# Performance work log

Hardware: AMD Instinct MI355X
Metric: run time of the kernel (lower is better)

The kernel has to match this reference:

```python
import jax, jax.numpy as jnp
import numpy as np

B, Q, C, N_PER, GS = 8, 2048, 256, 64, 8
H1, H2 = 256, 64
EPS = 1e-5


def make_grid():
    a = jnp.linspace(-0.1, 0.1, GS)
    gx, gy = jnp.meshgrid(a, a, indexing='ij')  # torch.meshgrid default 'ij'
    return jnp.stack([gx.reshape(-1), gy.reshape(-1)], axis=1)  # (n, 2)


def setup_inputs() -> dict:
    key = jax.random.key(0)
    ks = jax.random.split(key, 10)
    s = lambda k, shp, fan: jax.random.normal(k, shp, jnp.float32) / np.sqrt(fan)
    return {
        'tokens': jax.random.normal(ks[0], (B, Q, C), jnp.float32),
        'grid': make_grid(),
        'Wc': s(ks[1], (C, 3), C), 'bc': jnp.zeros((3,), jnp.float32),
        'W1': s(ks[2], (C + 2, H1), C + 2), 'b1': jnp.zeros((H1,), jnp.float32),
        'gamma1': jnp.ones((H1,), jnp.float32), 'beta1': jnp.zeros((H1,), jnp.float32),
        'W2': s(ks[3], (H1, H2), H1), 'b2': jnp.zeros((H2,), jnp.float32),
        'gamma2': jnp.ones((H2,), jnp.float32), 'beta2': jnp.zeros((H2,), jnp.float32),
        'W3': s(ks[4], (H2, 3), H2), 'b3': jnp.zeros((3,), jnp.float32),
    }


def batchnorm(x, gamma, beta):
    # BatchNorm1d in training mode: stats over batch (B*Q) and length (n) dims,
    # per channel (last axis here).
    mean = jnp.mean(x, axis=(0, 1, 2), keepdims=True)
    var = jnp.var(x, axis=(0, 1, 2), keepdims=True)
    return gamma * (x - mean) * jax.lax.rsqrt(var + EPS) + beta


def reference(tokens, grid, Wc, bc, W1, b1, gamma1, beta1, W2, b2, gamma2, beta2, W3, b3):
    coarse = tokens @ Wc + bc  # (B, Q, 3)
    # conv1 (1x1) on concat([tokens_expanded, grid]) == split matmul + broadcast add;
    # avoids materializing the (B,Q,n,C+2) concat explicitly.
    tok_part = tokens @ W1[:C]                 # (B, Q, H1)
    grid_part = grid @ W1[C:]                  # (n, H1)
    h = tok_part[:, :, None, :] + grid_part[None, None, :, :] + b1  # (B, Q, n, H1)
    h = jax.nn.relu(batchnorm(h, gamma1, beta1))
    h = jnp.einsum('bqnc,cd->bqnd', h, W2) + b2  # (B, Q, n, H2)
    h = jax.nn.relu(batchnorm(h, gamma2, beta2))
    disp = jnp.einsum('bqnc,cd->bqnd', h, W3) + b3  # (B, Q, n, 3)
    fine = (coarse[:, :, None, :] + disp).reshape(B, Q * N_PER, 3)
    return coarse, fine
```

## Files before the change

### kernel.cpp

```cpp
#include <hip/hip_runtime.h>
#include <hip/hip_bf16.h>

#define ROWS 16384
#define C_   256
#define H1_  256
#define H2_  64
#define EPSN 1e-5f

typedef __bf16 bf16x8 __attribute__((ext_vector_type(8)));
typedef __bf16 bf16x4 __attribute__((ext_vector_type(4)));
typedef float  f32x4  __attribute__((ext_vector_type(4)));

__global__ __launch_bounds__(256) void k0_pack(const float* __restrict__ W1,
                                               const float* __restrict__ W2,
                                               const float* __restrict__ W3,
                                               __bf16* __restrict__ W1p,
                                               __bf16* __restrict__ W2p,
                                               __bf16* __restrict__ W3p,
                                               float* __restrict__ zero_base) {
    int idx = blockIdx.x * 256 + threadIdx.x;
    if (idx < 65536) {
        int j = idx & 7, l = (idx >> 3) & 63, rest = idx >> 9;
        int ks = rest & 7, CT = rest >> 3;
        int k = ks * 32 + ((l >> 4) << 3) + j;
        int c = CT * 16 + (l & 15);
        W1p[idx] = (__bf16)W1[k * H1_ + c];
    } else {
        int i2 = idx - 65536;
        int j = i2 & 7, l = (i2 >> 3) & 63, rest = i2 >> 9;
        int ks = rest & 7, CK = rest >> 3;
        int k = ks * 32 + ((l >> 4) << 3) + j;
        int c2 = CK * 16 + (l & 15);
        W2p[i2] = (__bf16)W2[k * H2_ + c2];
    }
    if (idx < 1024) {
        int j = idx & 7, l = (idx >> 3) & 63, ks = idx >> 9;
        int k = ks * 32 + ((l >> 4) << 3) + j;
        int c = l & 15;
        W3p[idx] = (c < 3) ? (__bf16)W3[k * 3 + c] : (__bf16)0.f;
    }
    if (idx < 24576) zero_base[idx] = 0.0f;
}

__global__ __launch_bounds__(256) void kc(const float* __restrict__ tokens,
                                          const float* __restrict__ Wc,
                                          const float* __restrict__ bc,
                                          float* __restrict__ coarse) {
    int t = threadIdx.x, w = t >> 6, l = t & 63;
    int row = blockIdx.x * 4 + w;
    int c0 = l * 4;
    f32x4 tv = *(const f32x4*)(tokens + (size_t)row * C_ + c0);
    f32x4 w0 = *(const f32x4*)(Wc + c0 * 3);
    f32x4 w1 = *(const f32x4*)(Wc + c0 * 3 + 4);
    f32x4 w2 = *(const f32x4*)(Wc + c0 * 3 + 8);
    float wc[12] = {w0[0], w0[1], w0[2], w0[3], w1[0], w1[1], w1[2], w1[3],
                    w2[0], w2[1], w2[2], w2[3]};
    float p[3] = {0.f, 0.f, 0.f};
#pragma unroll
    for (int i = 0; i < 4; ++i)
#pragma unroll
        for (int j = 0; j < 3; ++j) p[j] = fmaf(tv[i], wc[i * 3 + j], p[j]);
#pragma unroll
    for (int off = 1; off < 64; off <<= 1) {
#pragma unroll
        for (int j = 0; j < 3; ++j) p[j] += __shfl_xor(p[j], off, 64);
    }
    if (l == 0) {
#pragma unroll
        for (int j = 0; j < 3; ++j) coarse[row * 3 + j] = p[j] + bc[j];
    }
}

__global__ __launch_bounds__(256) void k1a(const float* __restrict__ tokens,
                                           const __bf16* __restrict__ W1p,
                                           float* __restrict__ tokpart,
                                           float* __restrict__ p1s,
                                           float* __restrict__ p1q) {
    __shared__ __align__(16) __bf16 Al[16 * 264];
    int t = threadIdx.x, w = t >> 6, l = t & 63;
    int quad = l >> 4, col = l & 15;
    int rowbase = (blockIdx.x >> 1) * 16;
    int colhalf = blockIdx.x & 1;
    int slot = blockIdx.x & 31;

    bf16x8 bfr[16];
#pragma unroll
    for (int ctl = 0; ctl < 2; ++ctl)
#pragma unroll
        for (int ks = 0; ks < 8; ++ks) {
            int CT = colhalf * 8 + w * 2 + ctl;
            bfr[ctl * 8 + ks] = *(const bf16x8*)(W1p + (((CT * 8 + ks) * 64 + l) * 8));
        }

    {
        int r = t >> 4, cb = (t & 15) * 16;
        const float* src = tokens + (size_t)(rowbase + r) * C_ + cb;
        f32x4 t0 = *(const f32x4*)(src);
        f32x4 t1 = *(const f32x4*)(src + 4);
        f32x4 t2 = *(const f32x4*)(src + 8);
        f32x4 t3 = *(const f32x4*)(src + 12);
        bf16x8 v0, v1;
#pragma unroll
        for (int e = 0; e < 4; ++e) {
            v0[e] = (__bf16)t0[e]; v0[e + 4] = (__bf16)t1[e];
            v1[e] = (__bf16)t2[e]; v1[e + 4] = (__bf16)t3[e];
        }
        *(bf16x8*)(&Al[r * 264 + cb]) = v0;
        *(bf16x8*)(&Al[r * 264 + cb + 8]) = v1;
    }
    __syncthreads();

    bf16x8 af[8];
#pragma unroll
    for (int ks = 0; ks < 8; ++ks)
        af[ks] = *(const bf16x8*)(&Al[col * 264 + ks * 32 + quad * 8]);

#pragma unroll
    for (int ctl = 0; ctl < 2; ++ctl) {
        f32x4 acc = {0.f, 0.f, 0.f, 0.f};
#pragma unroll
        for (int ks = 0; ks < 8; ++ks)
            acc = __builtin_amdgcn_mfma_f32_16x16x32_bf16(af[ks], bfr[ctl * 8 + ks], acc, 0, 0, 0);
        int c = colhalf * 128 + w * 32 + ctl * 16 + col;
        float s = 0.f, q = 0.f;
#pragma unroll
        for (int rr = 0; rr < 4; ++rr) {
            float v = acc[rr];
            tokpart[(size_t)(rowbase + quad * 4 + rr) * C_ + c] = v;
            s += v; q += v * v;
        }
        s += __shfl_xor(s, 16, 64); s += __shfl_xor(s, 32, 64);
        q += __shfl_xor(q, 16, 64); q += __shfl_xor(q, 32, 64);
        if (l < 16) {
            int cc = colhalf * 128 + w * 32 + ctl * 16 + l;
            atomicAdd(p1s + slot * C_ + cc, s);
            atomicAdd(p1q + slot * C_ + cc, q);
        }
    }
}

__global__ void k1b(const float* __restrict__ grid, const float* __restrict__ W1,
                    const float* __restrict__ gamma1, const float* __restrict__ beta1,
                    const float* __restrict__ p1s, const float* __restrict__ p1q,
                    float* __restrict__ a1o, float* __restrict__ d1o) {
    int t = threadIdx.x;
    float S = 0.f, Qq = 0.f;
    for (int s = 0; s < 32; ++s) { S += p1s[s * C_ + t]; Qq += p1q[s * C_ + t]; }
    float mean_t = S / (float)ROWS;
    float var_t = Qq / (float)ROWS - mean_t * mean_t;
    float wx = W1[C_ * H1_ + t];
    float wy = W1[(C_ + 1) * H1_ + t];
    float mg = 0.f, qg = 0.f;
    for (int n = 0; n < 64; ++n) {
        float gv = grid[2 * n] * wx + grid[2 * n + 1] * wy;
        mg += gv; qg += gv * gv;
    }
    mg *= (1.f / 64.f);
    float var_g = qg * (1.f / 64.f) - mg * mg;
    float a1 = gamma1[t] * rsqrtf(var_t + var_g + EPSN);
    a1o[t] = a1;
    d1o[t] = beta1[t] - a1 * (mean_t + mg);
}

__global__ __launch_bounds__(256) void k2(const float* __restrict__ tokpart,
                                          const float* __restrict__ grid,
                                          const float* __restrict__ W1,
                                          const __bf16* __restrict__ W2p,
                                          const float* __restrict__ a1,
                                          const float* __restrict__ d1,
                                          const float* __restrict__ b2,
                                          float* __restrict__ p2s,
                                          float* __restrict__ p2q) {
    __shared__ __align__(16) __bf16 y1[64 * 264];
    int t = threadIdx.x, w = t >> 6, l = t & 63;
    int quad = l >> 4, col = l & 15;
    int wn = w >> 1, wc = w & 1;
    int c0 = (l & 31) * 8, nh = l >> 5;

    bf16x8 bfr[16];
#pragma unroll
    for (int ck = 0; ck < 2; ++ck)
#pragma unroll
        for (int ks = 0; ks < 8; ++ks)
            bfr[ck * 8 + ks] = *(const bf16x8*)(W2p + ((((wc * 2 + ck) * 8 + ks) * 64 + l) * 8));

    float A_[8];
#pragma unroll
    for (int j = 0; j < 8; ++j) A_[j] = grid[2 * j + 1];
    float wgx[8], wgy[8];
    {
        f32x4 a0 = *(const f32x4*)(a1 + c0), a1h = *(const f32x4*)(a1 + c0 + 4);
        f32x4 x0 = *(const f32x4*)(W1 + C_ * H1_ + c0), x1 = *(const f32x4*)(W1 + C_ * H1_ + c0 + 4);
        f32x4 y0 = *(const f32x4*)(W1 + (C_ + 1) * H1_ + c0), yh = *(const f32x4*)(W1 + (C_ + 1) * H1_ + c0 + 4);
#pragma unroll
        for (int e = 0; e < 4; ++e) {
            wgx[e] = a0[e] * x0[e]; wgx[e + 4] = a1h[e] * x1[e];
            wgy[e] = a0[e] * y0[e]; wgy[e + 4] = a1h[e] * yh[e];
        }
    }
    float b2v[2];
#pragma unroll
    for (int ck = 0; ck < 2; ++ck) b2v[ck] = b2[wc * 32 + ck * 16 + col];

    float s[2] = {0.f, 0.f}, q[2] = {0.f, 0.f};

#pragma unroll 1
    for (int r8 = 0; r8 < 8; ++r8) {
        int row = blockIdx.x * 8 + r8;
        float base[8];
        {
            f32x4 t0 = *(const f32x4*)(tokpart + (size_t)row * C_ + c0);
            f32x4 t1 = *(const f32x4*)(tokpart + (size_t)row * C_ + c0 + 4);
            f32x4 av0 = *(const f32x4*)(a1 + c0), av1 = *(const f32x4*)(a1 + c0 + 4);
            f32x4 dv0 = *(const f32x4*)(d1 + c0), dv1 = *(const f32x4*)(d1 + c0 + 4);
#pragma unroll
            for (int e = 0; e < 4; ++e) {
                base[e] = fmaf(av0[e], t0[e], dv0[e]);
                base[e + 4] = fmaf(av1[e], t1[e], dv1[e]);
            }
        }
#pragma unroll
        for (int ih = 0; ih < 2; ++ih) {
            float ax = A_[2 * w + ih];
            float tc[8];
#pragma unroll
            for (int e = 0; e < 8; ++e) tc[e] = fmaf(wgx[e], ax, base[e]);
#pragma unroll
            for (int kk = 0; kk < 4; ++kk) {
                int iy = nh + 2 * kk;
                float ay = A_[iy];
                int n = w * 16 + ih * 8 + iy;
                bf16x8 v;
#pragma unroll
                for (int e = 0; e < 8; ++e)
                    v[e] = (__bf16)fmaxf(fmaf(wgy[e], ay, tc[e]), 0.f);
                *(bf16x8*)(&y1[n * 264 + c0]) = v;
            }
        }
        __syncthreads();
#pragma unroll
        for (int rt = 0; rt < 2; ++rt) {
            bf16x8 af[8];
#pragma unroll
            for (int ks = 0; ks < 8; ++ks)
                af[ks] = *(const bf16x8*)(&y1[(wn * 32 + rt * 16 + col) * 264 + ks * 32 + quad * 8]);
#pragma unroll
            for (int ck = 0; ck < 2; ++ck) {
                f32x4 acc = {0.f, 0.f, 0.f, 0.f};
#pragma unroll
                for (int ks = 0; ks < 8; ++ks)
                    acc = __builtin_amdgcn_mfma_f32_16x16x32_bf16(af[ks], bfr[ck * 8 + ks], acc, 0, 0, 0);
#pragma unroll
                for (int rr = 0; rr < 4; ++rr) {
                    float h = acc[rr] + b2v[ck];
                    s[ck] += h; q[ck] += h * h;
                }
            }
        }
        __syncthreads();
    }
    int slot = blockIdx.x & 63;
#pragma unroll
    for (int ck = 0; ck < 2; ++ck) {
        float sv = s[ck], qv = q[ck];
        sv += __shfl_xor(sv, 16, 64); sv += __shfl_xor(sv, 32, 64);
        qv += __shfl_xor(qv, 16, 64); qv += __shfl_xor(qv, 32, 64);
        if (l < 16) {
            atomicAdd(p2s + slot * H2_ + wc * 32 + ck * 16 + l, sv);
            atomicAdd(p2q + slot * H2_ + wc * 32 + ck * 16 + l, qv);
        }
    }
}

__global__ void k2b(const float* __restrict__ p2s, const float* __restrict__ p2q,
                    const float* __restrict__ gamma2, const float* __restrict__ beta2,
                    const float* __restrict__ b2,
                    float* __restrict__ a2o, float* __restrict__ d2o) {
    int t = threadIdx.x;
    float S = 0.f, Qq = 0.f;
    for (int s = 0; s < 64; ++s) { S += p2s[s * H2_ + t]; Qq += p2q[s * H2_ + t]; }
    const float invN = 1.f / ((float)ROWS * 64.f);
    float mean = S * invN;
    float var = Qq * invN - mean * mean;
    float a2 = gamma2[t] * rsqrtf(var + EPSN);
    a2o[t] = a2;
    d2o[t] = beta2[t] - a2 * (mean - b2[t]);
}

__global__ __launch_bounds__(256) void k3(const float* __restrict__ tokpart,
                                          const float* __restrict__ grid,
                                          const float* __restrict__ W1,
                                          const __bf16* __restrict__ W2p,
                                          const float* __restrict__ a1,
                                          const float* __restrict__ d1,
                                          const __bf16* __restrict__ W3p,
                                          const float* __restrict__ a2,
                                          const float* __restrict__ d2p,
                                          const float* __restrict__ b3,
                                          const float* __restrict__ coarse,
                                          float* __restrict__ fine) {
    __shared__ __align__(16) __bf16 y1[64 * 264];
    __shared__ __align__(16) __bf16 y2l[64 * 72];
    __shared__ __align__(16) float finebuf[8 * 192];
    int t = threadIdx.x, w = t >> 6, l = t & 63;
    int quad = l >> 4, col = l & 15;
    int wn = w >> 1, wc = w & 1;
    int c0 = (l & 31) * 8, nh = l >> 5;

    bf16x8 bfr[16];
#pragma unroll
    for (int ck = 0; ck < 2; ++ck)
#pragma unroll
        for (int ks = 0; ks < 8; ++ks)
            bfr[ck * 8 + ks] = *(const bf16x8*)(W2p + ((((wc * 2 + ck) * 8 + ks) * 64 + l) * 8));
    bf16x8 wfr[2];
#pragma unroll
    for (int ks = 0; ks < 2; ++ks)
        wfr[ks] = *(const bf16x8*)(W3p + ((ks * 64 + l) * 8));

    float A_[8];
#pragma unroll
    for (int j = 0; j < 8; ++j) A_[j] = grid[2 * j + 1];
    float wgx[8], wgy[8];
    {
        f32x4 a0 = *(const f32x4*)(a1 + c0), a1h = *(const f32x4*)(a1 + c0 + 4);
        f32x4 x0 = *(const f32x4*)(W1 + C_ * H1_ + c0), x1 = *(const f32x4*)(W1 + C_ * H1_ + c0 + 4);
        f32x4 y0 = *(const f32x4*)(W1 + (C_ + 1) * H1_ + c0), yh = *(const f32x4*)(W1 + (C_ + 1) * H1_ + c0 + 4);
#pragma unroll
        for (int e = 0; e < 4; ++e) {
            wgx[e] = a0[e] * x0[e]; wgx[e + 4] = a1h[e] * x1[e];
            wgy[e] = a0[e] * y0[e]; wgy[e + 4] = a1h[e] * yh[e];
        }
    }
    float a2v[8], d2v[8];
#pragma unroll
    for (int ck = 0; ck < 2; ++ck)
#pragma unroll
        for (int rr = 0; rr < 4; ++rr) {
            int c2 = wc * 32 + ck * 16 + quad * 4 + rr;
            a2v[ck * 4 + rr] = a2[c2];
            d2v[ck * 4 + rr] = d2p[c2];
        }
    float b3v = (col < 3) ? b3[col] : 0.f;

#pragma unroll 1
    for (int r8 = 0; r8 < 8; ++r8) {
        int row = blockIdx.x * 8 + r8;
        float base[8];
        {
            f32x4 t0 = *(const f32x4*)(tokpart + (size_t)row * C_ + c0);
            f32x4 t1 = *(const f32x4*)(tokpart + (size_t)row * C_ + c0 + 4);
            f32x4 av0 = *(const f32x4*)(a1 + c0), av1 = *(const f32x4*)(a1 + c0 + 4);
            f32x4 dv0 = *(const f32x4*)(d1 + c0), dv1 = *(const f32x4*)(d1 + c0 + 4);
#pragma unroll
            for (int e = 0; e < 4; ++e) {
                base[e] = fmaf(av0[e], t0[e], dv0[e]);
                base[e + 4] = fmaf(av1[e], t1[e], dv1[e]);
            }
        }
#pragma unroll
        for (int ih = 0; ih < 2; ++ih) {
            float ax = A_[2 * w + ih];
            float tc[8];
#pragma unroll
            for (int e = 0; e < 8; ++e) tc[e] = fmaf(wgx[e], ax, base[e]);
#pragma unroll
            for (int kk = 0; kk < 4; ++kk) {
                int iy = nh + 2 * kk;
                float ay = A_[iy];
                int n = w * 16 + ih * 8 + iy;
                bf16x8 v;
#pragma unroll
                for (int e = 0; e < 8; ++e)
                    v[e] = (__bf16)fmaxf(fmaf(wgy[e], ay, tc[e]), 0.f);
                *(bf16x8*)(&y1[n * 264 + c0]) = v;
            }
        }
        __syncthreads();
#pragma unroll
        for (int rt = 0; rt < 2; ++rt) {
            bf16x8 af[8];
#pragma unroll
            for (int ks = 0; ks < 8; ++ks)
                af[ks] = *(const bf16x8*)(&y1[(wn * 32 + rt * 16 + col) * 264 + ks * 32 + quad * 8]);
#pragma unroll
            for (int ck = 0; ck < 2; ++ck) {
                f32x4 acc = {0.f, 0.f, 0.f, 0.f};
#pragma unroll
                for (int ks = 0; ks < 8; ++ks)
                    acc = __builtin_amdgcn_mfma_f32_16x16x32_bf16(bfr[ck * 8 + ks], af[ks], acc, 0, 0, 0);
                bf16x4 v;
#pragma unroll
                for (int rr = 0; rr < 4; ++rr)
                    v[rr] = (__bf16)fmaxf(fmaf(a2v[ck * 4 + rr], acc[rr], d2v[ck * 4 + rr]), 0.f);
                *(bf16x4*)(&y2l[(wn * 32 + rt * 16 + col) * 72 + wc * 32 + ck * 16 + quad * 4]) = v;
            }
        }
        __syncthreads();
        bf16x8 af2[2];
#pragma unroll
        for (int ks = 0; ks < 2; ++ks)
            af2[ks] = *(const bf16x8*)(&y2l[(w * 16 + col) * 72 + ks * 32 + quad * 8]);
        f32x4 d2acc = {0.f, 0.f, 0.f, 0.f};
        d2acc = __builtin_amdgcn_mfma_f32_16x16x32_bf16(af2[0], wfr[0], d2acc, 0, 0, 0);
        d2acc = __builtin_amdgcn_mfma_f32_16x16x32_bf16(af2[1], wfr[1], d2acc, 0, 0, 0);
        if (col < 3) {
            float cj = coarse[row * 3 + col] + b3v;
#pragma unroll
            for (int rr = 0; rr < 4; ++rr)
                finebuf[r8 * 192 + (w * 16 + quad * 4 + rr) * 3 + col] = d2acc[rr] + cj;
        }
    }
    __syncthreads();
    {
        float* dst = fine + (size_t)blockIdx.x * 1536;
        const f32x4* fb = (const f32x4*)finebuf;
        *(f32x4*)(dst + 4 * t) = fb[t];
        if (t < 128) *(f32x4*)(dst + 1024 + 4 * t) = fb[256 + t];
    }
}

extern "C" void kernel_launch(void* const* d_in, const int* in_sizes, int n_in,
                              void* d_out, int out_size, void* d_ws, size_t ws_size,
                              hipStream_t stream) {
    (void)in_sizes; (void)n_in; (void)out_size; (void)ws_size;
    const float* tokens = (const float*)d_in[0];
    const float* grid   = (const float*)d_in[1];
    const float* Wc     = (const float*)d_in[2];
    const float* bc     = (const float*)d_in[3];
    const float* W1     = (const float*)d_in[4];
    const float* gamma1 = (const float*)d_in[6];
    const float* beta1  = (const float*)d_in[7];
    const float* W2     = (const float*)d_in[8];
    const float* b2     = (const float*)d_in[9];
    const float* gamma2 = (const float*)d_in[10];
    const float* beta2  = (const float*)d_in[11];
    const float* W3     = (const float*)d_in[12];
    const float* b3     = (const float*)d_in[13];

    char* ws = (char*)d_ws;
    float*  tokpart = (float*)(ws);
    __bf16* W1p     = (__bf16*)(ws + 16777216);
    __bf16* W2p     = (__bf16*)(ws + 16908288);
    float*  p1s     = (float*)(ws + 16941056);
    float*  p1q     = (float*)(ws + 16973824);
    float*  p2s     = (float*)(ws + 17006592);
    float*  p2q     = (float*)(ws + 17022976);
    float*  a1      = (float*)(ws + 17039360);
    float*  d1      = (float*)(ws + 17040384);
    float*  a2      = (float*)(ws + 17041408);
    float*  d2p     = (float*)(ws + 17041664);
    __bf16* W3p     = (__bf16*)(ws + 17041920);

    float* coarse = (float*)d_out;
    float* fine   = (float*)d_out + (size_t)ROWS * 3;

    k0_pack<<<320, 256, 0, stream>>>(W1, W2, W3, W1p, W2p, W3p, p1s);
    kc<<<ROWS / 4, 256, 0, stream>>>(tokens, Wc, bc, coarse);
    k1a<<<2048, 256, 0, stream>>>(tokens, W1p, tokpart, p1s, p1q);
    k1b<<<1, 256, 0, stream>>>(grid, W1, gamma1, beta1, p1s, p1q, a1, d1);
    k2<<<ROWS / 8, 256, 0, stream>>>(tokpart, grid, W1, W2p, a1, d1, b2, p2s, p2q);
    k2b<<<1, 64, 0, stream>>>(p2s, p2q, gamma2, beta2, b2, a2, d2p);
    k3<<<ROWS / 8, 256, 0, stream>>>(tokpart, grid, W1, W2p, a1, d1, W3p, a2, d2p, b3, coarse, fine);
}
```

Before: 227.6 us.

## Spill layer-2 pre-activations to workspace to skip recompute in final pass

The second layer's pre-BN outputs (bf16) are written to a large workspace buffer during the statistics pass, so the final kernel can read them back instead of recomputing layer 1 and the W2 GEMM. This path is taken only when the workspace is large enough; otherwise the old recompute path runs. The coarse projection is also folded into k1a, removing a separate kernel. Packed bf16 conversions and a b2 cancellation in the BN algebra are added as well. The spill path trades recompute for roughly 128MB of extra global write and read traffic.

New measurement: 212.4 us. -6.7%, faster.

```diff
diff --git a/kernel.cpp b/kernel.cpp
--- a/kernel.cpp
+++ b/kernel.cpp
@@ -9,7 +9,17 @@
 
 typedef __bf16 bf16x8 __attribute__((ext_vector_type(8)));
 typedef __bf16 bf16x4 __attribute__((ext_vector_type(4)));
+typedef __bf16 bf16x2 __attribute__((ext_vector_type(2)));
 typedef float  f32x4  __attribute__((ext_vector_type(4)));
+typedef float  f32x2  __attribute__((ext_vector_type(2)));
+
+__device__ __forceinline__ bf16x2 cvt2(float a, float b) {
+#if __has_builtin(__builtin_amdgcn_cvt_pk_bf16_f32)
+    return __builtin_bit_cast(bf16x2, __builtin_amdgcn_cvt_pk_bf16_f32(a, b));
+#else
+    bf16x2 r; r[0] = (__bf16)a; r[1] = (__bf16)b; return r;
+#endif
+}
 
 __global__ __launch_bounds__(256) void k0_pack(const float* __restrict__ W1,
                                                const float* __restrict__ W2,
@@ -42,38 +52,73 @@
     if (idx < 24576) zero_base[idx] = 0.0f;
 }
 
-__global__ __launch_bounds__(256) void kc(const float* __restrict__ tokens,
-                                          const float* __restrict__ Wc,
-                                          const float* __restrict__ bc,
-                                          float* __restrict__ coarse) {
-    int t = threadIdx.x, w = t >> 6, l = t & 63;
-    int row = blockIdx.x * 4 + w;
-    int c0 = l * 4;
-    f32x4 tv = *(const f32x4*)(tokens + (size_t)row * C_ + c0);
-    f32x4 w0 = *(const f32x4*)(Wc + c0 * 3);
-    f32x4 w1 = *(const f32x4*)(Wc + c0 * 3 + 4);
-    f32x4 w2 = *(const f32x4*)(Wc + c0 * 3 + 8);
-    float wc[12] = {w0[0], w0[1], w0[2], w0[3], w1[0], w1[1], w1[2], w1[3],
-                    w2[0], w2[1], w2[2], w2[3]};
-    float p[3] = {0.f, 0.f, 0.f};
-#pragma unroll
-    for (int i = 0; i < 4; ++i)
-#pragma unroll
-        for (int j = 0; j < 3; ++j) p[j] = fmaf(tv[i], wc[i * 3 + j], p[j]);
-#pragma unroll
-    for (int off = 1; off < 64; off <<= 1) {
-#pragma unroll
-        for (int j = 0; j < 3; ++j) p[j] += __shfl_xor(p[j], off, 64);
-    }
-    if (l == 0) {
-#pragma unroll
-        for (int j = 0; j < 3; ++j) coarse[row * 3 + j] = p[j] + bc[j];
+__device__ __forceinline__ void prep_ctx(const float* __restrict__ grid,
+                                         const float* __restrict__ W1,
+                                         const float* __restrict__ a1p, int c0,
+                                         f32x2* wgx2, f32x2* wgy2, float* A_) {
+#pragma unroll
+    for (int j = 0; j < 8; ++j) A_[j] = grid[2 * j + 1];
+    f32x4 a0 = *(const f32x4*)(a1p + c0), a1h = *(const f32x4*)(a1p + c0 + 4);
+    f32x4 x0 = *(const f32x4*)(W1 + C_ * H1_ + c0), x1 = *(const f32x4*)(W1 + C_ * H1_ + c0 + 4);
+    f32x4 y0 = *(const f32x4*)(W1 + (C_ + 1) * H1_ + c0), yh = *(const f32x4*)(W1 + (C_ + 1) * H1_ + c0 + 4);
+    float av[8] = {a0[0], a0[1], a0[2], a0[3], a1h[0], a1h[1], a1h[2], a1h[3]};
+    float wx[8] = {x0[0], x0[1], x0[2], x0[3], x1[0], x1[1], x1[2], x1[3]};
+    float wy[8] = {y0[0], y0[1], y0[2], y0[3], yh[0], yh[1], yh[2], yh[3]};
+#pragma unroll
+    for (int e = 0; e < 4; ++e) {
+        wgx2[e][0] = av[2 * e] * wx[2 * e];     wgx2[e][1] = av[2 * e + 1] * wx[2 * e + 1];
+        wgy2[e][0] = av[2 * e] * wy[2 * e];     wgy2[e][1] = av[2 * e + 1] * wy[2 * e + 1];
+    }
+}
+
+__device__ __forceinline__ void stage16(__bf16* __restrict__ y1, int w, int c0, int nh,
+                                        const float* __restrict__ a1p,
+                                        const float* __restrict__ d1p,
+                                        const f32x2* wgx2, const f32x2* wgy2,
+                                        const float* A_,
+                                        const float* __restrict__ tokrow) {
+    f32x4 t0 = *(const f32x4*)(tokrow + c0);
+    f32x4 t1 = *(const f32x4*)(tokrow + c0 + 4);
+    f32x4 a0 = *(const f32x4*)(a1p + c0), a1h = *(const f32x4*)(a1p + c0 + 4);
+    f32x4 d0 = *(const f32x4*)(d1p + c0), d1h = *(const f32x4*)(d1p + c0 + 4);
+    f32x2 base2[4];
+    base2[0][0] = fmaf(a0[0], t0[0], d0[0]);  base2[0][1] = fmaf(a0[1], t0[1], d0[1]);
+    base2[1][0] = fmaf(a0[2], t0[2], d0[2]);  base2[1][1] = fmaf(a0[3], t0[3], d0[3]);
+    base2[2][0] = fmaf(a1h[0], t1[0], d1h[0]); base2[2][1] = fmaf(a1h[1], t1[1], d1h[1]);
+    base2[3][0] = fmaf(a1h[2], t1[2], d1h[2]); base2[3][1] = fmaf(a1h[3], t1[3], d1h[3]);
+#pragma unroll
+    for (int ih = 0; ih < 2; ++ih) {
+        float axs = A_[2 * w + ih];
+        f32x2 ax2 = {axs, axs};
+        f32x2 tc2[4];
+#pragma unroll
+        for (int e = 0; e < 4; ++e) tc2[e] = __builtin_elementwise_fma(wgx2[e], ax2, base2[e]);
+#pragma unroll
+        for (int kk = 0; kk < 4; ++kk) {
+            int iy = nh + 2 * kk;
+            float ays = A_[iy];
+            f32x2 ay2 = {ays, ays};
+            f32x2 z = {0.f, 0.f};
+            int n = w * 16 + ih * 8 + iy;
+            bf16x8 out;
+            bf16x2* o2 = (bf16x2*)&out;
+#pragma unroll
+            for (int e = 0; e < 4; ++e) {
+                f32x2 v = __builtin_elementwise_max(
+                    __builtin_elementwise_fma(wgy2[e], ay2, tc2[e]), z);
+                o2[e] = cvt2(v[0], v[1]);
+            }
+            *(bf16x8*)(&y1[n * 264 + c0]) = out;
+        }
     }
 }
 
 __global__ __launch_bounds__(256) void k1a(const float* __restrict__ tokens,
                                            const __bf16* __restrict__ W1p,
+                                           const float* __restrict__ Wc,
+                                           const float* __restrict__ bc,
                                            float* __restrict__ tokpart,
+                                           float* __restrict__ coarse,
                                            float* __restrict__ p1s,
                                            float* __restrict__ p1q) {
     __shared__ __align__(16) __bf16 Al[16 * 264];
@@ -91,7 +136,6 @@
             int CT = colhalf * 8 + w * 2 + ctl;
             bfr[ctl * 8 + ks] = *(const bf16x8*)(W1p + (((CT * 8 + ks) * 64 + l) * 8));
         }
-
     {
         int r = t >> 4, cb = (t & 15) * 16;
         const float* src = tokens + (size_t)(rowbase + r) * C_ + cb;
@@ -100,11 +144,11 @@
         f32x4 t2 = *(const f32x4*)(src + 8);
         f32x4 t3 = *(const f32x4*)(src + 12);
         bf16x8 v0, v1;
-#pragma unroll
-        for (int e = 0; e < 4; ++e) {
-            v0[e] = (__bf16)t0[e]; v0[e + 4] = (__bf16)t1[e];
-            v1[e] = (__bf16)t2[e]; v1[e + 4] = (__bf16)t3[e];
-        }
+        bf16x2* p0 = (bf16x2*)&v0; bf16x2* p1 = (bf16x2*)&v1;
+        p0[0] = cvt2(t0[0], t0[1]); p0[1] = cvt2(t0[2], t0[3]);
+        p0[2] = cvt2(t1[0], t1[1]); p0[3] = cvt2(t1[2], t1[3]);
+        p1[0] = cvt2(t2[0], t2[1]); p1[1] = cvt2(t2[2], t2[3]);
+        p1[2] = cvt2(t3[0], t3[1]); p1[3] = cvt2(t3[2], t3[3]);
         *(bf16x8*)(&Al[r * 264 + cb]) = v0;
         *(bf16x8*)(&Al[r * 264 + cb + 8]) = v1;
     }
@@ -135,6 +179,33 @@
             int cc = colhalf * 128 + w * 32 + ctl * 16 + l;
             atomicAdd(p1s + slot * C_ + cc, s);
             atomicAdd(p1q + slot * C_ + cc, q);
+        }
+    }
+    if (colhalf == 0) {
+        const f32x4* wcp = (const f32x4*)(Wc + l * 12);
+        f32x4 wa = wcp[0], wb = wcp[1], wv = wcp[2];
+        float wcl[12] = {wa[0], wa[1], wa[2], wa[3], wb[0], wb[1], wb[2], wb[3],
+                         wv[0], wv[1], wv[2], wv[3]};
+#pragma unroll
+        for (int rr = 0; rr < 4; ++rr) {
+            int r = w * 4 + rr;
+            bf16x4 tv4 = *(const bf16x4*)(&Al[r * 264 + l * 4]);
+            float p[3] = {0.f, 0.f, 0.f};
+#pragma unroll
+            for (int i = 0; i < 4; ++i) {
+                float tvf = (float)tv4[i];
+#pragma unroll
+                for (int j = 0; j < 3; ++j) p[j] = fmaf(tvf, wcl[i * 3 + j], p[j]);
+            }
+#pragma unroll
+            for (int off = 1; off < 64; off <<= 1)
+#pragma unroll
+                for (int j = 0; j < 3; ++j) p[j] += __shfl_xor(p[j], off, 64);
+            if (l == 0) {
+#pragma unroll
+                for (int j = 0; j < 3; ++j)
+                    coarse[(size_t)(rowbase + r) * 3 + j] = p[j] + bc[j];
+            }
         }
     }
 }
@@ -162,16 +233,18 @@
     d1o[t] = beta1[t] - a1 * (mean_t + mg);
 }
 
+template <bool SPILL>
 __global__ __launch_bounds__(256) void k2(const float* __restrict__ tokpart,
                                           const float* __restrict__ grid,
                                           const float* __restrict__ W1,
                                           const __bf16* __restrict__ W2p,
                                           const float* __restrict__ a1,
                                           const float* __restrict__ d1,
-                                          const float* __restrict__ b2,
                                           float* __restrict__ p2s,
-                                          float* __restrict__ p2q) {
+                                          float* __restrict__ p2q,
+                                          __bf16* __restrict__ h2s) {
     __shared__ __align__(16) __bf16 y1[64 * 264];
+    __shared__ __align__(16) __bf16 y2l[SPILL ? 64 * 72 : 8];
     int t = threadIdx.x, w = t >> 6, l = t & 63;
     int quad = l >> 4, col = l & 15;
     int wn = w >> 1, wc = w & 1;
@@ -184,59 +257,15 @@
         for (int ks = 0; ks < 8; ++ks)
             bfr[ck * 8 + ks] = *(const bf16x8*)(W2p + ((((wc * 2 + ck) * 8 + ks) * 64 + l) * 8));
 
-    float A_[8];
-#pragma unroll
-    for (int j = 0; j < 8; ++j) A_[j] = grid[2 * j + 1];
-    float wgx[8], wgy[8];
-    {
-        f32x4 a0 = *(const f32x4*)(a1 + c0), a1h = *(const f32x4*)(a1 + c0 + 4);
-        f32x4 x0 = *(const f32x4*)(W1 + C_ * H1_ + c0), x1 = *(const f32x4*)(W1 + C_ * H1_ + c0 + 4);
-        f32x4 y0 = *(const f32x4*)(W1 + (C_ + 1) * H1_ + c0), yh = *(const f32x4*)(W1 + (C_ + 1) * H1_ + c0 + 4);
-#pragma unroll
-        for (int e = 0; e < 4; ++e) {
-            wgx[e] = a0[e] * x0[e]; wgx[e + 4] = a1h[e] * x1[e];
-            wgy[e] = a0[e] * y0[e]; wgy[e + 4] = a1h[e] * yh[e];
-        }
-    }
-    float b2v[2];
-#pragma unroll
-    for (int ck = 0; ck < 2; ++ck) b2v[ck] = b2[wc * 32 + ck * 16 + col];
-
-    float s[2] = {0.f, 0.f}, q[2] = {0.f, 0.f};
+    f32x2 wgx2[4], wgy2[4]; float A_[8];
+    prep_ctx(grid, W1, a1, c0, wgx2, wgy2, A_);
+
+    float s[2][4] = {}, q[2][4] = {};
 
 #pragma unroll 1
     for (int r8 = 0; r8 < 8; ++r8) {
         int row = blockIdx.x * 8 + r8;
-        float base[8];
-        {
-            f32x4 t0 = *(const f32x4*)(tokpart + (size_t)row * C_ + c0);
-            f32x4 t1 = *(const f32x4*)(tokpart + (size_t)row * C_ + c0 + 4);
-            f32x4 av0 = *(const f32x4*)(a1 + c0), av1 = *(const f32x4*)(a1 + c0 + 4);
-            f32x4 dv0 = *(const f32x4*)(d1 + c0), dv1 = *(const f32x4*)(d1 + c0 + 4);
-#pragma unroll
-            for (int e = 0; e < 4; ++e) {
-                base[e] = fmaf(av0[e], t0[e], dv0[e]);
-                base[e + 4] = fmaf(av1[e], t1[e], dv1[e]);
-            }
-        }
-#pragma unroll
-        for (int ih = 0; ih < 2; ++ih) {
-            float ax = A_[2 * w + ih];
-            float tc[8];
-#pragma unroll
-            for (int e = 0; e < 8; ++e) tc[e] = fmaf(wgx[e], ax, base[e]);
-#pragma unroll
-            for (int kk = 0; kk < 4; ++kk) {
-                int iy = nh + 2 * kk;
-                float ay = A_[iy];
-                int n = w * 16 + ih * 8 + iy;
-                bf16x8 v;
-#pragma unroll
-                for (int e = 0; e < 8; ++e)
-                    v[e] = (__bf16)fmaxf(fmaf(wgy[e], ay, tc[e]), 0.f);
-                *(bf16x8*)(&y1[n * 264 + c0]) = v;
-            }
-        }
+        stage16(y1, w, c0, nh, a1, d1, wgx2, wgy2, A_, tokpart + (size_t)row * C_);
         __syncthreads();
 #pragma unroll
         for (int rt = 0; rt < 2; ++rt) {
@@ -249,32 +278,50 @@
                 f32x4 acc = {0.f, 0.f, 0.f, 0.f};
 #pragma unroll
                 for (int ks = 0; ks < 8; ++ks)
-                    acc = __builtin_amdgcn_mfma_f32_16x16x32_bf16(af[ks], bfr[ck * 8 + ks], acc, 0, 0, 0);
+                    acc = __builtin_amdgcn_mfma_f32_16x16x32_bf16(bfr[ck * 8 + ks], af[ks], acc, 0, 0, 0);
 #pragma unroll
                 for (int rr = 0; rr < 4; ++rr) {
-                    float h = acc[rr] + b2v[ck];
-                    s[ck] += h; q[ck] += h * h;
+                    s[ck][rr] += acc[rr];
+                    q[ck][rr] += acc[rr] * acc[rr];
+                }
+                if constexpr (SPILL) {
+                    bf16x4 v; bf16x2* v2 = (bf16x2*)&v;
+                    v2[0] = cvt2(acc[0], acc[1]);
+                    v2[1] = cvt2(acc[2], acc[3]);
+                    *(bf16x4*)(&y2l[(wn * 32 + rt * 16 + col) * 72 + wc * 32 + ck * 16 + quad * 4]) = v;
                 }
             }
         }
         __syncthreads();
+        if constexpr (SPILL) {
+            int n = t >> 2, cb = (t & 3) * 16;
+            bf16x8 u0 = *(const bf16x8*)(&y2l[n * 72 + cb]);
+            bf16x8 u1 = *(const bf16x8*)(&y2l[n * 72 + cb + 8]);
+            __bf16* dst = h2s + (size_t)row * 4096 + t * 16;
+            *(bf16x8*)dst = u0;
+            *(bf16x8*)(dst + 8) = u1;
+        }
     }
     int slot = blockIdx.x & 63;
 #pragma unroll
-    for (int ck = 0; ck < 2; ++ck) {
-        float sv = s[ck], qv = q[ck];
-        sv += __shfl_xor(sv, 16, 64); sv += __shfl_xor(sv, 32, 64);
-        qv += __shfl_xor(qv, 16, 64); qv += __shfl_xor(qv, 32, 64);
-        if (l < 16) {
-            atomicAdd(p2s + slot * H2_ + wc * 32 + ck * 16 + l, sv);
-            atomicAdd(p2q + slot * H2_ + wc * 32 + ck * 16 + l, qv);
-        }
-    }
+    for (int ck = 0; ck < 2; ++ck)
+#pragma unroll
+        for (int rr = 0; rr < 4; ++rr) {
+            float sv = s[ck][rr], qv = q[ck][rr];
+            sv += __shfl_xor(sv, 1, 64); sv += __shfl_xor(sv, 2, 64);
+            sv += __shfl_xor(sv, 4, 64); sv += __shfl_xor(sv, 8, 64);
+            qv += __shfl_xor(qv, 1, 64); qv += __shfl_xor(qv, 2, 64);
+            qv += __shfl_xor(qv, 4, 64); qv += __shfl_xor(qv, 8, 64);
+            if (col == 0) {
+                int c2 = wc * 32 + ck * 16 + quad * 4 + rr;
+                atomicAdd(p2s + slot * H2_ + c2, sv);
+                atomicAdd(p2q + slot * H2_ + c2, qv);
+            }
+        }
 }
 
 __global__ void k2b(const float* __restrict__ p2s, const float* __restrict__ p2q,
                     const float* __restrict__ gamma2, const float* __restrict__ beta2,
-                    const float* __restrict__ b2,
                     float* __restrict__ a2o, float* __restrict__ d2o) {
     int t = threadIdx.x;
     float S = 0.f, Qq = 0.f;
@@ -284,21 +331,93 @@
     float var = Qq * invN - mean * mean;
     float a2 = gamma2[t] * rsqrtf(var + EPSN);
     a2o[t] = a2;
-    d2o[t] = beta2[t] - a2 * (mean - b2[t]);
-}
-
-__global__ __launch_bounds__(256) void k3(const float* __restrict__ tokpart,
-                                          const float* __restrict__ grid,
-                                          const float* __restrict__ W1,
-                                          const __bf16* __restrict__ W2p,
-                                          const float* __restrict__ a1,
-                                          const float* __restrict__ d1,
-                                          const __bf16* __restrict__ W3p,
-                                          const float* __restrict__ a2,
-                                          const float* __restrict__ d2p,
-                                          const float* __restrict__ b3,
-                                          const float* __restrict__ coarse,
-                                          float* __restrict__ fine) {
+    d2o[t] = beta2[t] - a2 * mean;
+}
+
+__global__ __launch_bounds__(256) void k3s(const __bf16* __restrict__ h2s,
+                                           const float* __restrict__ a2,
+                                           const float* __restrict__ d2p,
+                                           const __bf16* __restrict__ W3p,
+                                           const float* __restrict__ b3,
+                                           const float* __restrict__ coarse,
+                                           float* __restrict__ fine) {
+    __shared__ __align__(16) __bf16 y2l[8][64 * 72];
+    __shared__ __align__(16) float finebuf[8 * 192];
+    int t = threadIdx.x, w = t >> 6, l = t & 63;
+    int quad = l >> 4, col = l & 15;
+
+    bf16x8 wfr[2];
+#pragma unroll
+    for (int ks = 0; ks < 2; ++ks)
+        wfr[ks] = *(const bf16x8*)(W3p + ((ks * 64 + l) * 8));
+
+    int n = t >> 2, cb = (t & 3) * 16;
+    float a2r[16], d2r[16];
+#pragma unroll
+    for (int i = 0; i < 16; i += 4) {
+        f32x4 av = *(const f32x4*)(a2 + cb + i);
+        f32x4 dv = *(const f32x4*)(d2p + cb + i);
+#pragma unroll
+        for (int e = 0; e < 4; ++e) { a2r[i + e] = av[e]; d2r[i + e] = dv[e]; }
+    }
+#pragma unroll 1
+    for (int r8 = 0; r8 < 8; ++r8) {
+        size_t row = (size_t)blockIdx.x * 8 + r8;
+        const __bf16* src = h2s + row * 4096 + t * 16;
+        bf16x8 u0 = *(const bf16x8*)src;
+        bf16x8 u1 = *(const bf16x8*)(src + 8);
+        bf16x8 o0, o1;
+        bf16x2* p0 = (bf16x2*)&o0; bf16x2* p1 = (bf16x2*)&o1;
+#pragma unroll
+        for (int e = 0; e < 4; ++e) {
+            p0[e] = cvt2(fmaxf(fmaf(a2r[2 * e],     (float)u0[2 * e],     d2r[2 * e]), 0.f),
+                         fmaxf(fmaf(a2r[2 * e + 1], (float)u0[2 * e + 1], d2r[2 * e + 1]), 0.f));
+            p1[e] = cvt2(fmaxf(fmaf(a2r[8 + 2 * e],     (float)u1[2 * e],     d2r[8 + 2 * e]), 0.f),
+                         fmaxf(fmaf(a2r[8 + 2 * e + 1], (float)u1[2 * e + 1], d2r[8 + 2 * e + 1]), 0.f));
+        }
+        *(bf16x8*)(&y2l[r8][n * 72 + cb]) = o0;
+        *(bf16x8*)(&y2l[r8][n * 72 + cb + 8]) = o1;
+    }
+    __syncthreads();
+    float b3v = (col < 3) ? b3[col] : 0.f;
+#pragma unroll 1
+    for (int r8 = 0; r8 < 8; ++r8) {
+        int row = blockIdx.x * 8 + r8;
+        bf16x8 af2[2];
+#pragma unroll
+        for (int ks = 0; ks < 2; ++ks)
+            af2[ks] = *(const bf16x8*)(&y2l[r8][(w * 16 + col) * 72 + ks * 32 + quad * 8]);
+        f32x4 acc = {0.f, 0.f, 0.f, 0.f};
+        acc = __builtin_amdgcn_mfma_f32_16x16x32_bf16(af2[0], wfr[0], acc, 0, 0, 0);
+        acc = __builtin_amdgcn_mfma_f32_16x16x32_bf16(af2[1], wfr[1], acc, 0, 0, 0);
+        if (col < 3) {
+            float cj = coarse[row * 3 + col] + b3v;
+#pragma unroll
+            for (int rr = 0; rr < 4; ++rr)
+                finebuf[r8 * 192 + (w * 16 + quad * 4 + rr) * 3 + col] = acc[rr] + cj;
+        }
+    }
+    __syncthreads();
+    {
+        float* dst = fine + (size_t)blockIdx.x * 1536;
+        const f32x4* fb = (const f32x4*)finebuf;
+        *(f32x4*)(dst + 4 * t) = fb[t];
+        if (t < 128) *(f32x4*)(dst + 1024 + 4 * t) = fb[256 + t];
+    }
+}
+
+__global__ __launch_bounds__(256) void k3r(const float* __restrict__ tokpart,
+                                           const float* __restrict__ grid,
+                                           const float* __restrict__ W1,
+                                           const __bf16* __restrict__ W2p,
+                                           const float* __restrict__ a1,
+                                           const float* __restrict__ d1,
+                                           const __bf16* __restrict__ W3p,
+                                           const float* __restrict__ a2,
+                                           const float* __restrict__ d2p,
+                                           const float* __restrict__ b3,
+                                           const float* __restrict__ coarse,
+                                           float* __restrict__ fine) {
     __shared__ __align__(16) __bf16 y1[64 * 264];
     __shared__ __align__(16) __bf16 y2l[64 * 72];
     __shared__ __align__(16) float finebuf[8 * 192];
@@ -318,20 +437,9 @@
     for (int ks = 0; ks < 2; ++ks)
         wfr[ks] = *(const bf16x8*)(W3p + ((ks * 64 + l) * 8));
 
-    float A_[8];
-#pragma unroll
-    for (int j = 0; j < 8; ++j) A_[j] = grid[2 * j + 1];
-    float wgx[8], wgy[8];
-    {
-        f32x4 a0 = *(const f32x4*)(a1 + c0), a1h = *(const f32x4*)(a1 + c0 + 4);
-        f32x4 x0 = *(const f32x4*)(W1 + C_ * H1_ + c0), x1 = *(const f32x4*)(W1 + C_ * H1_ + c0 + 4);
-        f32x4 y0 = *(const f32x4*)(W1 + (C_ + 1) * H1_ + c0), yh = *(const f32x4*)(W1 + (C_ + 1) * H1_ + c0 + 4);
-#pragma unroll
-        for (int e = 0; e < 4; ++e) {
-            wgx[e] = a0[e] * x0[e]; wgx[e + 4] = a1h[e] * x1[e];
-            wgy[e] = a0[e] * y0[e]; wgy[e + 4] = a1h[e] * yh[e];
-        }
-    }
+    f32x2 wgx2[4], wgy2[4]; float A_[8];
+    prep_ctx(grid, W1, a1, c0, wgx2, wgy2, A_);
+
     float a2v[8], d2v[8];
 #pragma unroll
     for (int ck = 0; ck < 2; ++ck)
@@ -346,36 +454,7 @@
 #pragma unroll 1
     for (int r8 = 0; r8 < 8; ++r8) {
         int row = blockIdx.x * 8 + r8;
-        float base[8];
-        {
-            f32x4 t0 = *(const f32x4*)(tokpart + (size_t)row * C_ + c0);
-            f32x4 t1 = *(const f32x4*)(tokpart + (size_t)row * C_ + c0 + 4);
-            f32x4 av0 = *(const f32x4*)(a1 + c0), av1 = *(const f32x4*)(a1 + c0 + 4);
-            f32x4 dv0 = *(const f32x4*)(d1 + c0), dv1 = *(const f32x4*)(d1 + c0 + 4);
-#pragma unroll
-            for (int e = 0; e < 4; ++e) {
-                base[e] = fmaf(av0[e], t0[e], dv0[e]);
-                base[e + 4] = fmaf(av1[e], t1[e], dv1[e]);
-            }
-        }
-#pragma unroll
-        for (int ih = 0; ih < 2; ++ih) {
-            float ax = A_[2 * w + ih];
-            float tc[8];
-#pragma unroll
-            for (int e = 0; e < 8; ++e) tc[e] = fmaf(wgx[e], ax, base[e]);
-#pragma unroll
-            for (int kk = 0; kk < 4; ++kk) {
-                int iy = nh + 2 * kk;
-                float ay = A_[iy];
-                int n = w * 16 + ih * 8 + iy;
-                bf16x8 v;
-#pragma unroll
-                for (int e = 0; e < 8; ++e)
-                    v[e] = (__bf16)fmaxf(fmaf(wgy[e], ay, tc[e]), 0.f);
-                *(bf16x8*)(&y1[n * 264 + c0]) = v;
-            }
-        }
+        stage16(y1, w, c0, nh, a1, d1, wgx2, wgy2, A_, tokpart + (size_t)row * C_);
         __syncthreads();
 #pragma unroll
         for (int rt = 0; rt < 2; ++rt) {
@@ -389,10 +468,12 @@
 #pragma unroll
                 for (int ks = 0; ks < 8; ++ks)
                     acc = __builtin_amdgcn_mfma_f32_16x16x32_bf16(bfr[ck * 8 + ks], af[ks], acc, 0, 0, 0);
-                bf16x4 v;
-#pragma unroll
-                for (int rr = 0; rr < 4; ++rr)
-                    v[rr] = (__bf16)fmaxf(fmaf(a2v[ck * 4 + rr], acc[rr], d2v[ck * 4 + rr]), 0.f);
+                bf16x4 v; bf16x2* v2 = (bf16x2*)&v;
+                float y0 = fmaxf(fmaf(a2v[ck * 4 + 0], acc[0], d2v[ck * 4 + 0]), 0.f);
+                float y1v = fmaxf(fmaf(a2v[ck * 4 + 1], acc[1], d2v[ck * 4 + 1]), 0.f);
+                float y2 = fmaxf(fmaf(a2v[ck * 4 + 2], acc[2], d2v[ck * 4 + 2]), 0.f);
+                float y3 = fmaxf(fmaf(a2v[ck * 4 + 3], acc[3], d2v[ck * 4 + 3]), 0.f);
+                v2[0] = cvt2(y0, y1v); v2[1] = cvt2(y2, y3);
                 *(bf16x4*)(&y2l[(wn * 32 + rt * 16 + col) * 72 + wc * 32 + ck * 16 + quad * 4]) = v;
             }
         }
@@ -423,7 +504,7 @@
 extern "C" void kernel_launch(void* const* d_in, const int* in_sizes, int n_in,
                               void* d_out, int out_size, void* d_ws, size_t ws_size,
                               hipStream_t stream) {
-    (void)in_sizes; (void)n_in; (void)out_size; (void)ws_size;
+    (void)in_sizes; (void)n_in; (void)out_size;
     const float* tokens = (const float*)d_in[0];
     const float* grid   = (const float*)d_in[1];
     const float* Wc     = (const float*)d_in[2];
@@ -432,34 +513,42 @@
     const float* gamma1 = (const float*)d_in[6];
     const float* beta1  = (const float*)d_in[7];
     const float* W2     = (const float*)d_in[8];
-    const float* b2     = (const float*)d_in[9];
     const float* gamma2 = (const float*)d_in[10];
     const float* beta2  = (const float*)d_in[11];
     const float* W3     = (const float*)d_in[12];
     const float* b3     = (const float*)d_in[13];
 
     char* ws = (char*)d_ws;
-    float*  tokpart = (float*)(ws);
-    __bf16* W1p     = (__bf16*)(ws + 16777216);
-    __bf16* W2p     = (__bf16*)(ws + 16908288);
-    float*  p1s     = (float*)(ws + 16941056);
-    float*  p1q     = (float*)(ws + 16973824);
-    float*  p2s     = (float*)(ws + 17006592);
-    float*  p2q     = (float*)(ws + 17022976);
-    float*  a1      = (float*)(ws + 17039360);
-    float*  d1      = (float*)(ws + 17040384);
-    float*  a2      = (float*)(ws + 17041408);
-    float*  d2p     = (float*)(ws + 17041664);
-    __bf16* W3p     = (__bf16*)(ws + 17041920);
+    __bf16* W1p     = (__bf16*)(ws);
+    __bf16* W2p     = (__bf16*)(ws + 131072);
+    float*  p1s     = (float*)(ws + 163840);
+    float*  p1q     = (float*)(ws + 196608);
+    float*  p2s     = (float*)(ws + 229376);
+    float*  p2q     = (float*)(ws + 245760);
+    float*  a1      = (float*)(ws + 262144);
+    float*  d1      = (float*)(ws + 263168);
+    float*  a2      = (float*)(ws + 264192);
+    float*  d2p     = (float*)(ws + 264448);
+    __bf16* W3p     = (__bf16*)(ws + 264704);
+    float*  tokpart = (float*)(ws + 266752);
+    __bf16* h2s     = (__bf16*)(ws + 17043968);
+
+    const size_t SPILL_NEED = 17043968ull + 134217728ull;
+    bool spill = ws_size >= SPILL_NEED;
 
     float* coarse = (float*)d_out;
     float* fine   = (float*)d_out + (size_t)ROWS * 3;
 
     k0_pack<<<320, 256, 0, stream>>>(W1, W2, W3, W1p, W2p, W3p, p1s);
-    kc<<<ROWS / 4, 256, 0, stream>>>(tokens, Wc, bc, coarse);
-    k1a<<<2048, 256, 0, stream>>>(tokens, W1p, tokpart, p1s, p1q);
+    k1a<<<2048, 256, 0, stream>>>(tokens, W1p, Wc, bc, tokpart, coarse, p1s, p1q);
     k1b<<<1, 256, 0, stream>>>(grid, W1, gamma1, beta1, p1s, p1q, a1, d1);
-    k2<<<ROWS / 8, 256, 0, stream>>>(tokpart, grid, W1, W2p, a1, d1, b2, p2s, p2q);
-    k2b<<<1, 64, 0, stream>>>(p2s, p2q, gamma2, beta2, b2, a2, d2p);
-    k3<<<ROWS / 8, 256, 0, stream>>>(tokpart, grid, W1, W2p, a1, d1, W3p, a2, d2p, b3, coarse, fine);
-}
+    if (spill) {
+        k2<true><<<ROWS / 8, 256, 0, stream>>>(tokpart, grid, W1, W2p, a1, d1, p2s, p2q, h2s);
+        k2b<<<1, 64, 0, stream>>>(p2s, p2q, gamma2, beta2, a2, d2p);
+        k3s<<<ROWS / 8, 256, 0, stream>>>(h2s, a2, d2p, W3p, b3, coarse, fine);
+    } else {
+        k2<false><<<ROWS / 8, 256, 0, stream>>>(tokpart, grid, W1, W2p, a1, d1, p2s, p2q, h2s);
+        k2b<<<1, 64, 0, stream>>>(p2s, p2q, gamma2, beta2, a2, d2p);
+        k3r<<<ROWS / 8, 256, 0, stream>>>(tokpart, grid, W1, W2p, a1, d1, W3p, a2, d2p, b3, coarse, fine);
+    }
+}
```
